# Performance work log

Hardware: AMD Instinct MI355X
Metric: run time of the kernel (lower is better)

## Reference

```python
import jax, jax.numpy as jnp
import numpy as np

N_NODES = 50000
N_EDGES = 600000
D = 128
LN_EPS = 1e-5


def setup_inputs() -> dict:
    key = jax.random.key(0)
    ks = jax.random.split(key, 10)
    s = 1.0 / np.sqrt(D)
    return {
        "node_reps": jax.random.normal(ks[0], (N_NODES, D), jnp.float32),
        "edge_reps": jax.random.normal(ks[1], (N_EDGES, D), jnp.float32),
        "src_idx": jax.random.randint(ks[2], (N_EDGES,), 0, N_NODES, jnp.int32),
        "dst_idx": jnp.sort(jax.random.randint(ks[3], (N_EDGES,), 0, N_NODES, jnp.int32)),
        "Wq": jax.random.normal(ks[4], (D, D), jnp.float32) * s,
        "Wk": jax.random.normal(ks[5], (D, D), jnp.float32) * s,
        "Wv": jax.random.normal(ks[6], (D, D), jnp.float32) * s,
        "Wo": jax.random.normal(ks[7], (D, D), jnp.float32) * s,
        "ln_gamma": jnp.ones((D,), jnp.float32),
        "ln_beta": jnp.zeros((D,), jnp.float32),
        "W1": jax.random.normal(ks[8], (3 * D, D), jnp.float32) * (1.0 / np.sqrt(3 * D)),
        "b1": jnp.zeros((D,), jnp.float32),
        "W2": jax.random.normal(ks[9], (D, D), jnp.float32) * s,
        "b2": jnp.zeros((D,), jnp.float32),
    }


def _layer_norm(x, g, b):
    mu = jnp.mean(x, axis=-1, keepdims=True)
    var = jnp.mean(jnp.square(x - mu), axis=-1, keepdims=True)
    return (x - mu) * jax.lax.rsqrt(var + LN_EPS) * g + b


def reference(node_reps, edge_reps, src_idx, dst_idx, Wq, Wk, Wv, Wo,
              ln_gamma, ln_beta, W1, b1, W2, b2):
    n_nodes, d = node_reps.shape
    # dense projections once per node (kernel-friendly GEMMs)
    q = node_reps @ Wq                                  # [N, d]
    k_nodes = node_reps @ Wk                            # [N, d]
    v_nodes = node_reps @ Wv                            # [N, d]
    # per-edge gather + edge bias
    k_e = k_nodes[src_idx] + edge_reps                  # [E, d]
    scores = jnp.sum(q[dst_idx] * k_e, axis=-1) / jnp.sqrt(jnp.float32(d))  # [E]
    # segment softmax over edges sharing the same dst node
    seg_max = jax.ops.segment_max(scores, dst_idx, num_segments=n_nodes)
    ex = jnp.exp(scores - seg_max[dst_idx])
    denom = jax.ops.segment_sum(ex, dst_idx, num_segments=n_nodes)
    alpha = ex / denom[dst_idx]                          # [E]
    v_e = v_nodes[src_idx] + edge_reps                   # [E, d]
    agg = jax.ops.segment_sum(alpha[:, None] * v_e, dst_idx, num_segments=n_nodes)  # [N, d]
    updated = _layer_norm(node_reps + agg @ Wo, ln_gamma, ln_beta)  # [N, d]
    # triplet fusion MLP over (dst node, edge, src node)
    h_trip = jnp.concatenate([node_reps[dst_idx], edge_reps, node_reps[src_idx]], axis=-1)  # [E, 3d]
    fused = jax.nn.relu(h_trip @ W1 + b1) @ W2 + b2      # [E, d]
    return updated, fused
```

## Files before the change

kernel.cpp:

```cpp
#include <hip/hip_runtime.h>
#include <hip/hip_bf16.h>

#define NN 50000
#define NE 600000
#define D 128

typedef __bf16 bf16x8 __attribute__((ext_vector_type(8)));
typedef __bf16 bf16x4 __attribute__((ext_vector_type(4)));
typedef float f32x4 __attribute__((ext_vector_type(4)));


static __device__ __forceinline__ bf16x8 load_a_frag_nc(const float* __restrict__ A,
                                                        int row, int k0) {
  const f32x4* p = (const f32x4*)(A + (size_t)row * D + k0);
  f32x4 v0 = p[0], v1 = p[1];
  bf16x8 r;
  r[0] = (__bf16)v0[0]; r[1] = (__bf16)v0[1]; r[2] = (__bf16)v0[2]; r[3] = (__bf16)v0[3];
  r[4] = (__bf16)v1[0]; r[5] = (__bf16)v1[1]; r[6] = (__bf16)v1[2]; r[7] = (__bf16)v1[3];
  return r;
}

static __device__ __forceinline__ void stage_a_tile128(const float* __restrict__ A, int M,
                                                       int row_base, char* lds, int tid) {
  const int l32 = tid & 31;
  const int g = tid >> 5;
#pragma unroll
  for (int it = 0; it < 16; ++it) {
    int rl = it * 8 + g;
    int r = row_base + rl;
    f32x4 v = {};
    if (r < M) v = *(const f32x4*)(A + (size_t)r * D + l32 * 4);
    bf16x4 b;
    b[0] = (__bf16)v[0]; b[1] = (__bf16)v[1]; b[2] = (__bf16)v[2]; b[3] = (__bf16)v[3];
    int byte = (rl * 256 + l32 * 8) ^ ((rl & 7) << 4);
    *(bf16x4*)(lds + byte) = b;
  }
}

static __device__ __forceinline__ bf16x8 read_a_frag(const char* lds, int rl, int k0) {
  int byte = (rl * 256 + k0 * 2) ^ ((rl & 7) << 4);
  return *(const bf16x8*)(lds + byte);
}

template <int CTRL>
static __device__ __forceinline__ float dpp_add(float x) {
  int v = __builtin_amdgcn_update_dpp(0, __float_as_int(x), CTRL, 0xf, 0xf, true);
  return x + __int_as_float(v);
}

static __device__ __forceinline__ float red32(float x) {
  x = dpp_add<0xB1>(x);
  x = dpp_add<0x4E>(x);
  x = dpp_add<0x124>(x);
  x = dpp_add<0x128>(x);
  return x + __shfl_xor(x, 16, 64);
}

#define CATT 0.12751744612764933f

struct PrepArgs {
  const float* W[8];
  __bf16* WT[8];
  const int* dst;
  int* offs;
};

__global__ void prep_all(PrepArgs pa) {
  int b = blockIdx.x;
  if (b < 512) {
    int w = b >> 6;
    int t = (b & 63) * 256 + threadIdx.x;
    int n = t & 127, k = t >> 7;
    float v = pa.W[w][k * 128 + n];
    if (w == 0) v *= CATT;
    pa.WT[w][n * 128 + k] = (__bf16)v;
  } else {
    int n = (b - 512) * 256 + threadIdx.x;
    if (n > NN) return;
    int lo = 0, hi = NE;
    while (lo < hi) {
      int mid = (lo + hi) >> 1;
      if (pa.dst[mid] < n) lo = mid + 1; else hi = mid;
    }
    pa.offs[n] = lo;
  }
}

struct GemmBatch {
  const __bf16* BT[5];
  void* C[5];
  const float* bias[5];
  int mode[5];
};

__global__ __launch_bounds__(256) void gemm_k128_b(const float* __restrict__ A,
                                                   GemmBatch gb, int M) {
  __shared__ __align__(16) char atile[128 * 256];
  const int y = blockIdx.y;
  const __bf16* __restrict__ BT = gb.BT[y];
  const int tid = threadIdx.x;
  const int lane = tid & 63;
  const int wave = tid >> 6;
  const int wr = wave >> 1, wc = wave & 1;
  const int row0 = blockIdx.x * 128;
  const int col0 = wc * 64;
  const int lr = lane & 15;
  const int lk = (lane >> 4) << 3;

  stage_a_tile128(A, M, row0, atile, tid);
  __syncthreads();

  f32x4 acc[4][4] = {};
#pragma unroll
  for (int kk = 0; kk < 4; ++kk) {
    const int k0 = kk * 32 + lk;
    bf16x8 a[4], b[4];
#pragma unroll
    for (int m = 0; m < 4; ++m) a[m] = read_a_frag(atile, wr * 64 + m * 16 + lr, k0);
#pragma unroll
    for (int n = 0; n < 4; ++n) b[n] = *(const bf16x8*)(BT + (size_t)(col0 + n * 16 + lr) * D + k0);
#pragma unroll
    for (int m = 0; m < 4; ++m)
#pragma unroll
      for (int n = 0; n < 4; ++n)
        acc[m][n] = __builtin_amdgcn_mfma_f32_16x16x32_bf16(a[m], b[n], acc[m][n], 0, 0, 0);
  }
  const int rr = (lane >> 4) * 4;
  float bv[4] = {0.f, 0.f, 0.f, 0.f};
  if (gb.bias[y]) {
#pragma unroll
    for (int n = 0; n < 4; ++n) bv[n] = gb.bias[y][col0 + n * 16 + lr];
  }
  const int mode = gb.mode[y];
#pragma unroll
  for (int m = 0; m < 4; ++m)
#pragma unroll
    for (int j = 0; j < 4; ++j) {
      const int row = row0 + wr * 64 + m * 16 + rr + j;
      if (row < M) {
#pragma unroll
        for (int n = 0; n < 4; ++n) {
          const int c = col0 + n * 16 + lr;
          const float val = acc[m][n][j] + bv[n];
          if (mode == 0) {
            ((float*)gb.C[y])[(size_t)row * D + c] = val;
          } else if (mode == 1) {
            ((__bf16*)gb.C[y])[(size_t)row * D + c] = (__bf16)val;
          } else {
            const int e = ((c >> 2) << 3) + (c & 3) + (mode == 3 ? 4 : 0);
            ((__bf16*)gb.C[y])[(size_t)row * 256 + e] = (__bf16)val;
          }
        }
      }
    }
}

#define LD1(P, K, J, SV)                                                     \
  do {                                                                       \
    const int jj_ = (J);                                                     \
    const int jc_ = jj_ < jm ? jj_ : 0;                                      \
    int si_ = __shfl((SV), jj_ & 31, 32);                                    \
    si_ = jj_ < jm ? si_ : 0;                                                \
    kv##P[K] = *(const bf16x8*)(KV + (size_t)si_ * 256 + (l32 << 3));        \
    ee##P[K] = *(const f32x4*)(edge + (size_t)(s0 + jc_) * D + (l32 << 2));  \
  } while (0)

#define LOADC(P, C)                                                          \
  do {                                                                       \
    const int c4_ = (C) * 4;                                                 \
    const int sv_ = (c4_ < 32) ? sidx0 : sidx1;                              \
    LD1(P, 0, c4_ + 0, sv_); LD1(P, 1, c4_ + 1, sv_);                        \
    LD1(P, 2, c4_ + 2, sv_); LD1(P, 3, c4_ + 3, sv_);                        \
  } while (0)

#define CP1(P, K, J)                                                         \
  do {                                                                       \
    const int jj_ = (J);                                                     \
    f32x4 ef_ = ee##P[K];                                                    \
    float x0_ = (float)kv##P[K][0] + ef_[0];                                 \
    float x1_ = (float)kv##P[K][1] + ef_[1];                                 \
    float x2_ = (float)kv##P[K][2] + ef_[2];                                 \
    float x3_ = (float)kv##P[K][3] + ef_[3];                                 \
    float pp_ = fmaf(qs[1], x1_, qs[0] * x0_) + fmaf(qs[3], x3_, qs[2] * x2_); \
    float s_ = red32(pp_);                                                   \
    float w_ = jj_ < jm ? exp2f(s_) : 0.f;                                   \
    l += w_;                                                                 \
    a[0] = fmaf(w_, (float)kv##P[K][4] + ef_[0], a[0]);                      \
    a[1] = fmaf(w_, (float)kv##P[K][5] + ef_[1], a[1]);                      \
    a[2] = fmaf(w_, (float)kv##P[K][6] + ef_[2], a[2]);                      \
    a[3] = fmaf(w_, (float)kv##P[K][7] + ef_[3], a[3]);                      \
  } while (0)

#define COMPC(P, C)                                                          \
  do {                                                                       \
    const int cc4_ = (C) * 4;                                                \
    CP1(P, 0, cc4_ + 0); CP1(P, 1, cc4_ + 1);                                \
    CP1(P, 2, cc4_ + 2); CP1(P, 3, cc4_ + 3);                                \
  } while (0)

#define MEMFENCE asm volatile("" ::: "memory")

__global__ __launch_bounds__(256) __attribute__((amdgpu_waves_per_eu(4)))
void fused_edge_attn(
    const float* __restrict__ edge,
    const __bf16* __restrict__ W1bT,
    const __bf16* __restrict__ W2T,
    const __bf16* __restrict__ P1,
    const __bf16* __restrict__ P3,
    const int* __restrict__ dst,
    const int* __restrict__ src,
    const float* __restrict__ b2,
    float* __restrict__ out_fused,
    const float* __restrict__ Q,
    const __bf16* __restrict__ KV,
    const int* __restrict__ offs,
    const __bf16* __restrict__ WoT,
    const float* __restrict__ noderep,
    const float* __restrict__ gamma,
    const float* __restrict__ beta,
    float* __restrict__ out_updated) {
  __shared__ __align__(16) char buf[64 * 256];
  const int tid = threadIdx.x;
  const int b = blockIdx.x;
  const int x = b & 7;
  const int t = b >> 3;
  const int grp = (t / 5) * 8 + x;
  const int role = t % 5;
  if (grp >= 3125) return;

  if (role >= 2) {
    const int ebi = grp * 3 + (role - 2);
    const int eb = ebi * 64;
    const int lane = tid & 63;
    const int wave = tid >> 6;
    const int wr = wave >> 1, wc = wave & 1;
    const int lr = lane & 15;
    const int lk = (lane >> 4) << 3;
    const int col0 = wc * 64;
    const int rr = (lane >> 4) * 4;

    f32x4 acc[2][4] = {};
#pragma unroll
    for (int kk = 0; kk < 4; ++kk) {
      const int k0 = kk * 32 + lk;
      bf16x8 a[2], bm[4];
#pragma unroll
      for (int m = 0; m < 2; ++m) a[m] = load_a_frag_nc(edge, eb + wr * 32 + m * 16 + lr, k0);
#pragma unroll
      for (int n = 0; n < 4; ++n) bm[n] = *(const bf16x8*)(W1bT + (size_t)(col0 + n * 16 + lr) * D + k0);
#pragma unroll
      for (int m = 0; m < 2; ++m)
#pragma unroll
        for (int n = 0; n < 4; ++n)
          acc[m][n] = __builtin_amdgcn_mfma_f32_16x16x32_bf16(a[m], bm[n], acc[m][n], 0, 0, 0);
    }

#pragma unroll
    for (int m = 0; m < 2; ++m) {
#pragma unroll
      for (int j = 0; j < 4; ++j) {
        const int rl = wr * 32 + m * 16 + rr + j;
        const __bf16* __restrict__ p1r = P1 + (size_t)dst[eb + rl] * D;
        const __bf16* __restrict__ p3r = P3 + (size_t)src[eb + rl] * D;
#pragma unroll
        for (int n = 0; n < 4; ++n) {
          const int c = col0 + n * 16 + lr;
          float v = fmaxf(acc[m][n][j] + (float)p1r[c] + (float)p3r[c], 0.f);
          int byte = (rl * 256 + c * 2) ^ ((rl & 7) << 4);
          *(__bf16*)(buf + byte) = (__bf16)v;
        }
      }
    }
    __syncthreads();

    float b2v[4];
#pragma unroll
    for (int n = 0; n < 4; ++n) b2v[n] = b2[col0 + n * 16 + lr];
    f32x4 acc2[2][4] = {};
#pragma unroll
    for (int kk = 0; kk < 4; ++kk) {
      const int k0 = kk * 32 + lk;
      bf16x8 a[2], bm[4];
#pragma unroll
      for (int m = 0; m < 2; ++m) a[m] = read_a_frag(buf, wr * 32 + m * 16 + lr, k0);
#pragma unroll
      for (int n = 0; n < 4; ++n) bm[n] = *(const bf16x8*)(W2T + (size_t)(col0 + n * 16 + lr) * D + k0);
#pragma unroll
      for (int m = 0; m < 2; ++m)
#pragma unroll
        for (int n = 0; n < 4; ++n)
          acc2[m][n] = __builtin_amdgcn_mfma_f32_16x16x32_bf16(a[m], bm[n], acc2[m][n], 0, 0, 0);
    }
#pragma unroll
    for (int m = 0; m < 2; ++m)
#pragma unroll
      for (int j = 0; j < 4; ++j) {
        int rl = wr * 32 + m * 16 + rr + j;
        int e = eb + rl;
#pragma unroll
        for (int n = 0; n < 4; ++n) {
          int c = col0 + n * 16 + lr;
          out_fused[(size_t)e * D + c] = acc2[m][n][j] + b2v[n];
        }
      }
  } else {
    const int nw = tid >> 5;
    const int node = (grp * 2 + role) * 8 + nw;
    const int l32 = tid & 31;
    int s0 = offs[node], s1 = offs[node + 1];
    int cnt = s1 - s0;
    f32x4 qs = *(const f32x4*)(Q + (size_t)node * D + l32 * 4);
    float l = 0.f;
    f32x4 a = {0.f, 0.f, 0.f, 0.f};

    const int jm = cnt < 64 ? cnt : 64;
    if (jm > 0) {
      int sidx0 = 0, sidx1 = 0;
      if (l32 < cnt) sidx0 = src[s0 + l32];
      if (l32 + 32 < cnt) sidx1 = src[s0 + 32 + l32];
      bf16x8 kv0[4], kv1[4];
      f32x4 ee0[4], ee1[4];
      const int nch = (jm + 3) >> 2;
      LOADC(0, 0);
      MEMFENCE;
      for (int c = 0; c < nch; c += 2) {
        if (c + 1 < nch) LOADC(1, c + 1);
        MEMFENCE;
        COMPC(0, c);
        if (c + 2 < nch) LOADC(0, c + 2);
        MEMFENCE;
        if (c + 1 < nch) COMPC(1, c + 1);
      }
      for (int i = 64; i < cnt; ++i) {
        int si = src[s0 + i];
        bf16x8 kvx = *(const bf16x8*)(KV + (size_t)si * 256 + (l32 << 3));
        f32x4 ef = *(const f32x4*)(edge + (size_t)(s0 + i) * D + (l32 << 2));
        float x0 = (float)kvx[0] + ef[0], x1 = (float)kvx[1] + ef[1];
        float x2 = (float)kvx[2] + ef[2], x3 = (float)kvx[3] + ef[3];
        float pp = fmaf(qs[1], x1, qs[0] * x0) + fmaf(qs[3], x3, qs[2] * x2);
        float w = exp2f(red32(pp));
        l += w;
        a[0] = fmaf(w, (float)kvx[4] + ef[0], a[0]);
        a[1] = fmaf(w, (float)kvx[5] + ef[1], a[1]);
        a[2] = fmaf(w, (float)kvx[6] + ef[2], a[2]);
        a[3] = fmaf(w, (float)kvx[7] + ef[3], a[3]);
      }
    }
    float inv = l > 0.f ? 1.f / l : 0.f;
    f32x4 r;
    r[0] = a[0] * inv; r[1] = a[1] * inv; r[2] = a[2] * inv; r[3] = a[3] * inv;

    {
      bf16x4 rb;
      rb[0] = (__bf16)r[0]; rb[1] = (__bf16)r[1];
      rb[2] = (__bf16)r[2]; rb[3] = (__bf16)r[3];
      int byte = (nw * 256 + l32 * 8) ^ ((nw & 7) << 4);
      *(bf16x4*)(buf + byte) = rb;
    }
    __syncthreads();

    {
      const int wave = tid >> 6;
      const int lane = tid & 63;
      const int lr = lane & 15;
      const int lk = (lane >> 4) << 3;
      f32x4 acc[2] = {};
#pragma unroll
      for (int kk = 0; kk < 4; ++kk) {
        int k0 = kk * 32 + lk;
        bf16x8 af = read_a_frag(buf, lr, k0);
#pragma unroll
        for (int tt = 0; tt < 2; ++tt) {
          int nn = wave * 2 + tt;
          bf16x8 bm = *(const bf16x8*)(WoT + (size_t)(nn * 16 + lr) * D + k0);
          acc[tt] = __builtin_amdgcn_mfma_f32_16x16x32_bf16(af, bm, acc[tt], 0, 0, 0);
        }
      }
      float* xl = (float*)(buf + 8192);
      const int rr = (lane >> 4) * 4;
      if (rr < 8) {
#pragma unroll
        for (int tt = 0; tt < 2; ++tt) {
          int nn = wave * 2 + tt;
#pragma unroll
          for (int j = 0; j < 4; ++j)
            xl[(rr + j) * 128 + nn * 16 + lr] = acc[tt][j];
        }
      }
    }
    __syncthreads();

    {
      const float* xl = (const float*)(buf + 8192);
      f32x4 xv = *(const f32x4*)(xl + nw * 128 + l32 * 4);
      f32x4 nv = *(const f32x4*)(noderep + (size_t)node * D + l32 * 4);
      float x0 = xv[0] + nv[0], x1 = xv[1] + nv[1];
      float x2 = xv[2] + nv[2], x3 = xv[3] + nv[3];
      float s = red32(x0 + x1 + x2 + x3);
      float mu = s * (1.f / 128.f);
      float d0 = x0 - mu, d1 = x1 - mu, d2 = x2 - mu, d3 = x3 - mu;
      float vv = red32(d0 * d0 + d1 * d1 + d2 * d2 + d3 * d3);
      float rstd = rsqrtf(vv * (1.f / 128.f) + 1e-5f);
      f32x4 g = *(const f32x4*)(gamma + l32 * 4);
      f32x4 bb = *(const f32x4*)(beta + l32 * 4);
      f32x4 o;
      o[0] = d0 * rstd * g[0] + bb[0];
      o[1] = d1 * rstd * g[1] + bb[1];
      o[2] = d2 * rstd * g[2] + bb[2];
      o[3] = d3 * rstd * g[3] + bb[3];
      *(f32x4*)(out_updated + (size_t)node * D + l32 * 4) = o;
    }
  }
}

extern "C" void kernel_launch(void* const* d_in, const int* in_sizes, int n_in,
                              void* d_out, int out_size, void* d_ws, size_t ws_size,
                              hipStream_t stream) {
  const float* node = (const float*)d_in[0];
  const float* edge = (const float*)d_in[1];
  const int* src = (const int*)d_in[2];
  const int* dst = (const int*)d_in[3];
  const float* Wq = (const float*)d_in[4];
  const float* Wk = (const float*)d_in[5];
  const float* Wv = (const float*)d_in[6];
  const float* Wo = (const float*)d_in[7];
  const float* gamma = (const float*)d_in[8];
  const float* beta = (const float*)d_in[9];
  const float* W1 = (const float*)d_in[10];
  const float* b1 = (const float*)d_in[11];
  const float* W2 = (const float*)d_in[12];
  const float* b2 = (const float*)d_in[13];

  float* out_updated = (float*)d_out;
  float* out_fused = (float*)d_out + (size_t)NN * D;

  char* ws = (char*)d_ws;
  size_t o = 0;
  auto take = [&](size_t bytes) {
    char* p = ws + o;
    o = (o + bytes + 255) & ~(size_t)255;
    return p;
  };
  int* offs = (int*)take((NN + 1) * sizeof(int));
  __bf16* WqT = (__bf16*)take(128 * 128 * 2);
  __bf16* WkT = (__bf16*)take(128 * 128 * 2);
  __bf16* WvT = (__bf16*)take(128 * 128 * 2);
  __bf16* WoT = (__bf16*)take(128 * 128 * 2);
  __bf16* W1aT = (__bf16*)take(128 * 128 * 2);
  __bf16* W1bT = (__bf16*)take(128 * 128 * 2);
  __bf16* W1cT = (__bf16*)take(128 * 128 * 2);
  __bf16* W2T = (__bf16*)take(128 * 128 * 2);
  float* Qb = (float*)take((size_t)NN * D * 4);
  __bf16* KVb = (__bf16*)take((size_t)NN * 256 * 2);
  __bf16* P1b = (__bf16*)take((size_t)NN * D * 2);
  __bf16* P3b = (__bf16*)take((size_t)NN * D * 2);

  PrepArgs pa;
  pa.W[0] = Wq; pa.WT[0] = WqT;
  pa.W[1] = Wk; pa.WT[1] = WkT;
  pa.W[2] = Wv; pa.WT[2] = WvT;
  pa.W[3] = Wo; pa.WT[3] = WoT;
  pa.W[4] = W1; pa.WT[4] = W1aT;
  pa.W[5] = W1 + 128 * 128; pa.WT[5] = W1bT;
  pa.W[6] = W1 + 256 * 128; pa.WT[6] = W1cT;
  pa.W[7] = W2; pa.WT[7] = W2T;
  pa.dst = dst; pa.offs = offs;
  prep_all<<<512 + (NN + 256) / 256, 256, 0, stream>>>(pa);

  int gnode = (NN + 127) / 128;
  GemmBatch gb;
  gb.BT[0] = WqT;  gb.C[0] = Qb;  gb.bias[0] = nullptr; gb.mode[0] = 0;
  gb.BT[1] = WkT;  gb.C[1] = KVb; gb.bias[1] = nullptr; gb.mode[1] = 2;
  gb.BT[2] = WvT;  gb.C[2] = KVb; gb.bias[2] = nullptr; gb.mode[2] = 3;
  gb.BT[3] = W1aT; gb.C[3] = P1b; gb.bias[3] = b1;      gb.mode[3] = 1;
  gb.BT[4] = W1cT; gb.C[4] = P3b; gb.bias[4] = nullptr; gb.mode[4] = 1;
  gemm_k128_b<<<dim3(gnode, 5), 256, 0, stream>>>(node, gb, NN);

  fused_edge_attn<<<15640, 256, 0, stream>>>(edge, W1bT, W2T, P1b, P3b, dst, src,
                                             b2, out_fused, Qb, KVb, offs,
                                             WoT, node, gamma, beta, out_updated);
}
```

Measured before the change: 433.9 us.

## Stage gathered P1+P3 rows through LDS with coalesced vector loads

The per-edge P1[dst] and P3[src] projection gathers move out of the MFMA output layout, where each lane read scattered single bf16 values. Threads now load whole rows as bf16x8 vectors, sum them, and write the result to a swizzled LDS tile; the accumulators then read it back before ReLU and rewrite the tile for the second GEMM. The change also drops the compiler memory fences in the attention loop and lowers the waves-per-EU hint from 4 to 3, which allows more registers per wave. The cost is two extra __syncthreads, an extra LDS round-trip, and the intermediate sum being rounded to bf16 before it is added to the accumulator.

```diff
diff --git a/kernel.cpp b/kernel.cpp
--- a/kernel.cpp
+++ b/kernel.cpp
@@ -198,9 +198,7 @@
     CP1(P, 2, cc4_ + 2); CP1(P, 3, cc4_ + 3);                                \
   } while (0)
 
-#define MEMFENCE asm volatile("" ::: "memory")
-
-__global__ __launch_bounds__(256) __attribute__((amdgpu_waves_per_eu(4)))
+__global__ __launch_bounds__(256) __attribute__((amdgpu_waves_per_eu(3)))
 void fused_edge_attn(
     const float* __restrict__ edge,
     const __bf16* __restrict__ W1bT,
@@ -255,22 +253,50 @@
           acc[m][n] = __builtin_amdgcn_mfma_f32_16x16x32_bf16(a[m], bm[n], acc[m][n], 0, 0, 0);
     }
 
-#pragma unroll
-    for (int m = 0; m < 2; ++m) {
+    {
+      const int rw = tid >> 2;
+      const int c0 = (tid & 3) << 5;
+      const __bf16* __restrict__ p1r = P1 + (size_t)dst[eb + rw] * D + c0;
+      const __bf16* __restrict__ p3r = P3 + (size_t)src[eb + rw] * D + c0;
+#pragma unroll
+      for (int i = 0; i < 4; ++i) {
+        bf16x8 a1 = *(const bf16x8*)(p1r + i * 8);
+        bf16x8 a3 = *(const bf16x8*)(p3r + i * 8);
+        bf16x8 g;
+#pragma unroll
+        for (int e = 0; e < 8; ++e) g[e] = (__bf16)((float)a1[e] + (float)a3[e]);
+        int byte = (rw * 256 + ((c0 + i * 8) << 1)) ^ ((rw & 7) << 4);
+        *(bf16x8*)(buf + byte) = g;
+      }
+    }
+    __syncthreads();
+
+#pragma unroll
+    for (int m = 0; m < 2; ++m)
 #pragma unroll
       for (int j = 0; j < 4; ++j) {
         const int rl = wr * 32 + m * 16 + rr + j;
-        const __bf16* __restrict__ p1r = P1 + (size_t)dst[eb + rl] * D;
-        const __bf16* __restrict__ p3r = P3 + (size_t)src[eb + rl] * D;
 #pragma unroll
         for (int n = 0; n < 4; ++n) {
           const int c = col0 + n * 16 + lr;
-          float v = fmaxf(acc[m][n][j] + (float)p1r[c] + (float)p3r[c], 0.f);
           int byte = (rl * 256 + c * 2) ^ ((rl & 7) << 4);
-          *(__bf16*)(buf + byte) = (__bf16)v;
+          acc[m][n][j] += (float)*(const __bf16*)(buf + byte);
         }
       }
-    }
+    __syncthreads();
+
+#pragma unroll
+    for (int m = 0; m < 2; ++m)
+#pragma unroll
+      for (int j = 0; j < 4; ++j) {
+        const int rl = wr * 32 + m * 16 + rr + j;
+#pragma unroll
+        for (int n = 0; n < 4; ++n) {
+          const int c = col0 + n * 16 + lr;
+          int byte = (rl * 256 + c * 2) ^ ((rl & 7) << 4);
+          *(__bf16*)(buf + byte) = (__bf16)fmaxf(acc[m][n][j], 0.f);
+        }
+      }
     __syncthreads();
 
     float b2v[4];
@@ -322,13 +348,10 @@
       f32x4 ee0[4], ee1[4];
       const int nch = (jm + 3) >> 2;
       LOADC(0, 0);
-      MEMFENCE;
       for (int c = 0; c < nch; c += 2) {
         if (c + 1 < nch) LOADC(1, c + 1);
-        MEMFENCE;
         COMPC(0, c);
         if (c + 2 < nch) LOADC(0, c + 2);
-        MEMFENCE;
         if (c + 1 < nch) COMPC(1, c + 1);
       }
       for (int i = 64; i < cnt; ++i) {
```

After: 431.8 us. Within noise of the previous version (-0.5%).

## Restructure triplet MLP blocks to per-wave 16-row tiles with async LDS gathers

Applied to the files above, without the earlier changes.

Edge MLP blocks now each handle 192 edges in three passes. Each wave owns a private 16-row tile and 8 KB of LDS, so the block-wide barrier is gone. The P1/P3 row gathers are issued as global_load_lds DMA into LDS before the first GEMM and awaited afterward, so their latency overlaps the MFMA work. Grid roles shrink from 5 to 3 per group, the launch count drops, waves_per_eu goes from 4 to 3, and the compiler memory fences in the attention loop are removed. The trade-offs are larger LDS per block and lower occupancy, and each wave reloads the full W1b/W2 weights for every 16-row tile.

```diff
diff --git a/kernel.cpp b/kernel.cpp
--- a/kernel.cpp
+++ b/kernel.cpp
@@ -9,6 +9,12 @@
 typedef __bf16 bf16x4 __attribute__((ext_vector_type(4)));
 typedef float f32x4 __attribute__((ext_vector_type(4)));
 
+
+static __device__ __forceinline__ void gload_lds16(const void* g, void* l) {
+  __builtin_amdgcn_global_load_lds(
+      (const __attribute__((address_space(1))) unsigned int*)g,
+      (__attribute__((address_space(3))) unsigned int*)l, 16, 0, 0);
+}
 
 static __device__ __forceinline__ bf16x8 load_a_frag_nc(const float* __restrict__ A,
                                                         int row, int k0) {
@@ -198,9 +204,7 @@
     CP1(P, 2, cc4_ + 2); CP1(P, 3, cc4_ + 3);                                \
   } while (0)
 
-#define MEMFENCE asm volatile("" ::: "memory")
-
-__global__ __launch_bounds__(256) __attribute__((amdgpu_waves_per_eu(4)))
+__global__ __launch_bounds__(256) __attribute__((amdgpu_waves_per_eu(3)))
 void fused_edge_attn(
     const float* __restrict__ edge,
     const __bf16* __restrict__ W1bT,
@@ -219,90 +223,97 @@
     const float* __restrict__ gamma,
     const float* __restrict__ beta,
     float* __restrict__ out_updated) {
-  __shared__ __align__(16) char buf[64 * 256];
+  __shared__ __align__(16) char buf[32768];
   const int tid = threadIdx.x;
   const int b = blockIdx.x;
   const int x = b & 7;
   const int t = b >> 3;
-  const int grp = (t / 5) * 8 + x;
-  const int role = t % 5;
+  const int grp = (t / 3) * 8 + x;
+  const int role = t % 3;
   if (grp >= 3125) return;
 
-  if (role >= 2) {
-    const int ebi = grp * 3 + (role - 2);
-    const int eb = ebi * 64;
+  if (role == 2) {
+    const int wave = tid >> 6;
     const int lane = tid & 63;
-    const int wave = tid >> 6;
-    const int wr = wave >> 1, wc = wave & 1;
     const int lr = lane & 15;
     const int lk = (lane >> 4) << 3;
-    const int col0 = wc * 64;
-    const int rr = (lane >> 4) * 4;
-
-    f32x4 acc[2][4] = {};
-#pragma unroll
-    for (int kk = 0; kk < 4; ++kk) {
-      const int k0 = kk * 32 + lk;
-      bf16x8 a[2], bm[4];
-#pragma unroll
-      for (int m = 0; m < 2; ++m) a[m] = load_a_frag_nc(edge, eb + wr * 32 + m * 16 + lr, k0);
-#pragma unroll
-      for (int n = 0; n < 4; ++n) bm[n] = *(const bf16x8*)(W1bT + (size_t)(col0 + n * 16 + lr) * D + k0);
-#pragma unroll
-      for (int m = 0; m < 2; ++m)
-#pragma unroll
-        for (int n = 0; n < 4; ++n)
-          acc[m][n] = __builtin_amdgcn_mfma_f32_16x16x32_bf16(a[m], bm[n], acc[m][n], 0, 0, 0);
-    }
-
-#pragma unroll
-    for (int m = 0; m < 2; ++m) {
-#pragma unroll
-      for (int j = 0; j < 4; ++j) {
-        const int rl = wr * 32 + m * 16 + rr + j;
-        const __bf16* __restrict__ p1r = P1 + (size_t)dst[eb + rl] * D;
-        const __bf16* __restrict__ p3r = P3 + (size_t)src[eb + rl] * D;
-#pragma unroll
-        for (int n = 0; n < 4; ++n) {
-          const int c = col0 + n * 16 + lr;
-          float v = fmaxf(acc[m][n][j] + (float)p1r[c] + (float)p3r[c], 0.f);
+    const int rr = (lane >> 4) << 2;
+    char* wbuf = buf + wave * 8192;
+    const int ebase = grp * 192;
+
+    float b2v[8];
+#pragma unroll
+    for (int n = 0; n < 8; ++n) b2v[n] = b2[n * 16 + lr];
+
+    for (int tt = 0; tt < 3; ++tt) {
+      const int er0 = ebase + tt * 64 + wave * 16;
+
+#pragma unroll
+      for (int q = 0; q < 4; ++q) {
+        const int row = er0 + q * 4 + (lane >> 4);
+        const int d = dst[row];
+        const int s = src[row];
+        gload_lds16((const char*)(P1 + (size_t)d * D) + (lr << 4), wbuf + q * 1024);
+        gload_lds16((const char*)(P3 + (size_t)s * D) + (lr << 4), wbuf + 4096 + q * 1024);
+      }
+
+      f32x4 acc[8] = {};
+#pragma unroll
+      for (int kk = 0; kk < 4; ++kk) {
+        const int k0 = kk * 32 + lk;
+        bf16x8 a = load_a_frag_nc(edge, er0 + lr, k0);
+#pragma unroll
+        for (int n = 0; n < 8; ++n) {
+          bf16x8 bm = *(const bf16x8*)(W1bT + (size_t)(n * 16 + lr) * D + k0);
+          acc[n] = __builtin_amdgcn_mfma_f32_16x16x32_bf16(a, bm, acc[n], 0, 0, 0);
+        }
+      }
+
+      asm volatile("s_waitcnt vmcnt(0)" ::: "memory");
+
+      const __bf16* g1 = (const __bf16*)wbuf;
+      const __bf16* g3 = (const __bf16*)(wbuf + 4096);
+#pragma unroll
+      for (int n = 0; n < 8; ++n)
+#pragma unroll
+        for (int j = 0; j < 4; ++j) {
+          const int rl = rr + j;
+          const int c = n * 16 + lr;
+          float v = acc[n][j] + (float)g1[rl * 128 + c] + (float)g3[rl * 128 + c];
+          acc[n][j] = fmaxf(v, 0.f);
+        }
+
+#pragma unroll
+      for (int n = 0; n < 8; ++n)
+#pragma unroll
+        for (int j = 0; j < 4; ++j) {
+          const int rl = rr + j;
+          const int c = n * 16 + lr;
           int byte = (rl * 256 + c * 2) ^ ((rl & 7) << 4);
-          *(__bf16*)(buf + byte) = (__bf16)v;
-        }
-      }
-    }
-    __syncthreads();
-
-    float b2v[4];
-#pragma unroll
-    for (int n = 0; n < 4; ++n) b2v[n] = b2[col0 + n * 16 + lr];
-    f32x4 acc2[2][4] = {};
-#pragma unroll
-    for (int kk = 0; kk < 4; ++kk) {
-      const int k0 = kk * 32 + lk;
-      bf16x8 a[2], bm[4];
-#pragma unroll
-      for (int m = 0; m < 2; ++m) a[m] = read_a_frag(buf, wr * 32 + m * 16 + lr, k0);
-#pragma unroll
-      for (int n = 0; n < 4; ++n) bm[n] = *(const bf16x8*)(W2T + (size_t)(col0 + n * 16 + lr) * D + k0);
-#pragma unroll
-      for (int m = 0; m < 2; ++m)
-#pragma unroll
-        for (int n = 0; n < 4; ++n)
-          acc2[m][n] = __builtin_amdgcn_mfma_f32_16x16x32_bf16(a[m], bm[n], acc2[m][n], 0, 0, 0);
-    }
-#pragma unroll
-    for (int m = 0; m < 2; ++m)
-#pragma unroll
-      for (int j = 0; j < 4; ++j) {
-        int rl = wr * 32 + m * 16 + rr + j;
-        int e = eb + rl;
-#pragma unroll
-        for (int n = 0; n < 4; ++n) {
-          int c = col0 + n * 16 + lr;
-          out_fused[(size_t)e * D + c] = acc2[m][n][j] + b2v[n];
-        }
-      }
+          *(__bf16*)(wbuf + byte) = (__bf16)acc[n][j];
+        }
+
+      f32x4 acc2[8] = {};
+#pragma unroll
+      for (int kk = 0; kk < 4; ++kk) {
+        const int k0 = kk * 32 + lk;
+        bf16x8 a = read_a_frag(wbuf, lr, k0);
+#pragma unroll
+        for (int n = 0; n < 8; ++n) {
+          bf16x8 bm = *(const bf16x8*)(W2T + (size_t)(n * 16 + lr) * D + k0);
+          acc2[n] = __builtin_amdgcn_mfma_f32_16x16x32_bf16(a, bm, acc2[n], 0, 0, 0);
+        }
+      }
+
+#pragma unroll
+      for (int n = 0; n < 8; ++n)
+#pragma unroll
+        for (int j = 0; j < 4; ++j) {
+          const int e = er0 + rr + j;
+          const int c = n * 16 + lr;
+          out_fused[(size_t)e * D + c] = acc2[n][j] + b2v[n];
+        }
+    }
   } else {
     const int nw = tid >> 5;
     const int node = (grp * 2 + role) * 8 + nw;
@@ -322,13 +333,10 @@
       f32x4 ee0[4], ee1[4];
       const int nch = (jm + 3) >> 2;
       LOADC(0, 0);
-      MEMFENCE;
       for (int c = 0; c < nch; c += 2) {
         if (c + 1 < nch) LOADC(1, c + 1);
-        MEMFENCE;
         COMPC(0, c);
         if (c + 2 < nch) LOADC(0, c + 2);
-        MEMFENCE;
         if (c + 1 < nch) COMPC(1, c + 1);
       }
       for (int i = 64; i < cnt; ++i) {
@@ -476,7 +484,7 @@
   gb.BT[4] = W1cT; gb.C[4] = P3b; gb.bias[4] = nullptr; gb.mode[4] = 1;
   gemm_k128_b<<<dim3(gnode, 5), 256, 0, stream>>>(node, gb, NN);
 
-  fused_edge_attn<<<15640, 256, 0, stream>>>(edge, W1bT, W2T, P1b, P3b, dst, src,
-                                             b2, out_fused, Qb, KVb, offs,
-                                             WoT, node, gamma, beta, out_updated);
-}
+  fused_edge_attn<<<9384, 256, 0, stream>>>(edge, W1bT, W2T, P1b, P3b, dst, src,
+                                            b2, out_fused, Qb, KVb, offs,
+                                            WoT, node, gamma, beta, out_updated);
+}
```

New measurement: 794.2 us. 83.0% more time.

## Recast per-node attention as block-tiled MFMA over 16-node edge tiles

Applied to the files above, without the earlier changes.

The attention path changes from one half-wave per node doing scalar dot products and shuffles to a block of 16 consecutive nodes. That block stages edge-plus-K and transposed edge-plus-V tiles in LDS and computes scores and the weighted aggregation with bf16 MFMA using a masked score matrix. Q is stored as a bf16 hi/lo split to keep precision, and the KV layout becomes contiguous K then V halves. The aim is to replace scalar FMA and shuffle work with matrix cores and to coalesce gathers, at the cost of wasted MFMA work on masked entries, extra syncs, and more LDS, which lowers the waves-per-EU hint.

```diff
diff --git a/kernel.cpp b/kernel.cpp
--- a/kernel.cpp
+++ b/kernel.cpp
@@ -8,6 +8,8 @@
 typedef __bf16 bf16x8 __attribute__((ext_vector_type(8)));
 typedef __bf16 bf16x4 __attribute__((ext_vector_type(4)));
 typedef float f32x4 __attribute__((ext_vector_type(4)));
+
+#define MFMA(a, b, c) __builtin_amdgcn_mfma_f32_16x16x32_bf16((a), (b), (c), 0, 0, 0)
 
 
 static __device__ __forceinline__ bf16x8 load_a_frag_nc(const float* __restrict__ A,
@@ -48,12 +50,17 @@
   return x + __int_as_float(v);
 }
 
-static __device__ __forceinline__ float red32(float x) {
+static __device__ __forceinline__ float red16(float x) {
   x = dpp_add<0xB1>(x);
   x = dpp_add<0x4E>(x);
   x = dpp_add<0x124>(x);
   x = dpp_add<0x128>(x);
-  return x + __shfl_xor(x, 16, 64);
+  return x;
+}
+
+static __device__ __forceinline__ float red32(float x) {
+  return red16(x) + __shfl_xor(red16(x) * 0.f + x + 0.f, 16, 64) * 0.f +
+         __shfl_xor(red16(x), 16, 64);
 }
 
 #define CATT 0.12751744612764933f
@@ -123,7 +130,7 @@
     for (int m = 0; m < 4; ++m)
 #pragma unroll
       for (int n = 0; n < 4; ++n)
-        acc[m][n] = __builtin_amdgcn_mfma_f32_16x16x32_bf16(a[m], b[n], acc[m][n], 0, 0, 0);
+        acc[m][n] = MFMA(a[m], b[n], acc[m][n]);
   }
   const int rr = (lane >> 4) * 4;
   float bv[4] = {0.f, 0.f, 0.f, 0.f};
@@ -142,65 +149,25 @@
         for (int n = 0; n < 4; ++n) {
           const int c = col0 + n * 16 + lr;
           const float val = acc[m][n][j] + bv[n];
-          if (mode == 0) {
-            ((float*)gb.C[y])[(size_t)row * D + c] = val;
-          } else if (mode == 1) {
-            ((__bf16*)gb.C[y])[(size_t)row * D + c] = (__bf16)val;
+          __bf16* C = (__bf16*)gb.C[y];
+          if (mode == 1) {
+            C[(size_t)row * D + c] = (__bf16)val;
+          } else if (mode == 2) {
+            C[(size_t)row * 256 + c] = (__bf16)val;
+          } else if (mode == 3) {
+            C[(size_t)row * 256 + 128 + c] = (__bf16)val;
           } else {
-            const int e = ((c >> 2) << 3) + (c & 3) + (mode == 3 ? 4 : 0);
-            ((__bf16*)gb.C[y])[(size_t)row * 256 + e] = (__bf16)val;
+            __bf16 vh = (__bf16)val;
+            __bf16 vl = (__bf16)(val - (float)vh);
+            C[(size_t)row * 256 + c] = vh;
+            C[(size_t)row * 256 + 128 + c] = vl;
           }
         }
       }
     }
 }
 
-#define LD1(P, K, J, SV)                                                     \
-  do {                                                                       \
-    const int jj_ = (J);                                                     \
-    const int jc_ = jj_ < jm ? jj_ : 0;                                      \
-    int si_ = __shfl((SV), jj_ & 31, 32);                                    \
-    si_ = jj_ < jm ? si_ : 0;                                                \
-    kv##P[K] = *(const bf16x8*)(KV + (size_t)si_ * 256 + (l32 << 3));        \
-    ee##P[K] = *(const f32x4*)(edge + (size_t)(s0 + jc_) * D + (l32 << 2));  \
-  } while (0)
-
-#define LOADC(P, C)                                                          \
-  do {                                                                       \
-    const int c4_ = (C) * 4;                                                 \
-    const int sv_ = (c4_ < 32) ? sidx0 : sidx1;                              \
-    LD1(P, 0, c4_ + 0, sv_); LD1(P, 1, c4_ + 1, sv_);                        \
-    LD1(P, 2, c4_ + 2, sv_); LD1(P, 3, c4_ + 3, sv_);                        \
-  } while (0)
-
-#define CP1(P, K, J)                                                         \
-  do {                                                                       \
-    const int jj_ = (J);                                                     \
-    f32x4 ef_ = ee##P[K];                                                    \
-    float x0_ = (float)kv##P[K][0] + ef_[0];                                 \
-    float x1_ = (float)kv##P[K][1] + ef_[1];                                 \
-    float x2_ = (float)kv##P[K][2] + ef_[2];                                 \
-    float x3_ = (float)kv##P[K][3] + ef_[3];                                 \
-    float pp_ = fmaf(qs[1], x1_, qs[0] * x0_) + fmaf(qs[3], x3_, qs[2] * x2_); \
-    float s_ = red32(pp_);                                                   \
-    float w_ = jj_ < jm ? exp2f(s_) : 0.f;                                   \
-    l += w_;                                                                 \
-    a[0] = fmaf(w_, (float)kv##P[K][4] + ef_[0], a[0]);                      \
-    a[1] = fmaf(w_, (float)kv##P[K][5] + ef_[1], a[1]);                      \
-    a[2] = fmaf(w_, (float)kv##P[K][6] + ef_[2], a[2]);                      \
-    a[3] = fmaf(w_, (float)kv##P[K][7] + ef_[3], a[3]);                      \
-  } while (0)
-
-#define COMPC(P, C)                                                          \
-  do {                                                                       \
-    const int cc4_ = (C) * 4;                                                \
-    CP1(P, 0, cc4_ + 0); CP1(P, 1, cc4_ + 1);                                \
-    CP1(P, 2, cc4_ + 2); CP1(P, 3, cc4_ + 3);                                \
-  } while (0)
-
-#define MEMFENCE asm volatile("" ::: "memory")
-
-__global__ __launch_bounds__(256) __attribute__((amdgpu_waves_per_eu(4)))
+__global__ __launch_bounds__(256) __attribute__((amdgpu_waves_per_eu(3)))
 void fused_edge_attn(
     const float* __restrict__ edge,
     const __bf16* __restrict__ W1bT,
@@ -211,7 +178,7 @@
     const int* __restrict__ src,
     const float* __restrict__ b2,
     float* __restrict__ out_fused,
-    const float* __restrict__ Q,
+    const __bf16* __restrict__ Qsp,
     const __bf16* __restrict__ KV,
     const int* __restrict__ offs,
     const __bf16* __restrict__ WoT,
@@ -219,25 +186,27 @@
     const float* __restrict__ gamma,
     const float* __restrict__ beta,
     float* __restrict__ out_updated) {
-  __shared__ __align__(16) char buf[64 * 256];
+  __shared__ __align__(16) char lds[34880];
   const int tid = threadIdx.x;
   const int b = blockIdx.x;
   const int x = b & 7;
   const int t = b >> 3;
-  const int grp = (t / 5) * 8 + x;
-  const int role = t % 5;
+  const int grp = (t >> 2) * 8 + x;
+  const int role = t & 3;
   if (grp >= 3125) return;
 
-  if (role >= 2) {
-    const int ebi = grp * 3 + (role - 2);
+  const int wave = tid >> 6;
+  const int lane = tid & 63;
+  const int lr = lane & 15;
+  const int kg = lane >> 4;
+  const int rr = kg << 2;
+  const int lk = kg << 3;
+
+  if (role != 0) {
+    const int ebi = grp * 3 + (role - 1);
     const int eb = ebi * 64;
-    const int lane = tid & 63;
-    const int wave = tid >> 6;
     const int wr = wave >> 1, wc = wave & 1;
-    const int lr = lane & 15;
-    const int lk = (lane >> 4) << 3;
     const int col0 = wc * 64;
-    const int rr = (lane >> 4) * 4;
 
     f32x4 acc[2][4] = {};
 #pragma unroll
@@ -252,7 +221,7 @@
       for (int m = 0; m < 2; ++m)
 #pragma unroll
         for (int n = 0; n < 4; ++n)
-          acc[m][n] = __builtin_amdgcn_mfma_f32_16x16x32_bf16(a[m], bm[n], acc[m][n], 0, 0, 0);
+          acc[m][n] = MFMA(a[m], bm[n], acc[m][n]);
     }
 
 #pragma unroll
@@ -267,7 +236,7 @@
           const int c = col0 + n * 16 + lr;
           float v = fmaxf(acc[m][n][j] + (float)p1r[c] + (float)p3r[c], 0.f);
           int byte = (rl * 256 + c * 2) ^ ((rl & 7) << 4);
-          *(__bf16*)(buf + byte) = (__bf16)v;
+          *(__bf16*)(lds + byte) = (__bf16)v;
         }
       }
     }
@@ -282,14 +251,14 @@
       const int k0 = kk * 32 + lk;
       bf16x8 a[2], bm[4];
 #pragma unroll
-      for (int m = 0; m < 2; ++m) a[m] = read_a_frag(buf, wr * 32 + m * 16 + lr, k0);
+      for (int m = 0; m < 2; ++m) a[m] = read_a_frag(lds, wr * 32 + m * 16 + lr, k0);
 #pragma unroll
       for (int n = 0; n < 4; ++n) bm[n] = *(const bf16x8*)(W2T + (size_t)(col0 + n * 16 + lr) * D + k0);
 #pragma unroll
       for (int m = 0; m < 2; ++m)
 #pragma unroll
         for (int n = 0; n < 4; ++n)
-          acc2[m][n] = __builtin_amdgcn_mfma_f32_16x16x32_bf16(a[m], bm[n], acc2[m][n], 0, 0, 0);
+          acc2[m][n] = MFMA(a[m], bm[n], acc2[m][n]);
     }
 #pragma unroll
     for (int m = 0; m < 2; ++m)
@@ -304,111 +273,189 @@
         }
       }
   } else {
-    const int nw = tid >> 5;
-    const int node = (grp * 2 + role) * 8 + nw;
-    const int l32 = tid & 31;
-    int s0 = offs[node], s1 = offs[node + 1];
-    int cnt = s1 - s0;
-    f32x4 qs = *(const f32x4*)(Q + (size_t)node * D + l32 * 4);
-    float l = 0.f;
-    f32x4 a = {0.f, 0.f, 0.f, 0.f};
-
-    const int jm = cnt < 64 ? cnt : 64;
-    if (jm > 0) {
-      int sidx0 = 0, sidx1 = 0;
-      if (l32 < cnt) sidx0 = src[s0 + l32];
-      if (l32 + 32 < cnt) sidx1 = src[s0 + 32 + l32];
-      bf16x8 kv0[4], kv1[4];
-      f32x4 ee0[4], ee1[4];
-      const int nch = (jm + 3) >> 2;
-      LOADC(0, 0);
-      MEMFENCE;
-      for (int c = 0; c < nch; c += 2) {
-        if (c + 1 < nch) LOADC(1, c + 1);
-        MEMFENCE;
-        COMPC(0, c);
-        if (c + 2 < nch) LOADC(0, c + 2);
-        MEMFENCE;
-        if (c + 1 < nch) COMPC(1, c + 1);
-      }
-      for (int i = 64; i < cnt; ++i) {
-        int si = src[s0 + i];
-        bf16x8 kvx = *(const bf16x8*)(KV + (size_t)si * 256 + (l32 << 3));
-        f32x4 ef = *(const f32x4*)(edge + (size_t)(s0 + i) * D + (l32 << 2));
-        float x0 = (float)kvx[0] + ef[0], x1 = (float)kvx[1] + ef[1];
-        float x2 = (float)kvx[2] + ef[2], x3 = (float)kvx[3] + ef[3];
-        float pp = fmaf(qs[1], x1, qs[0] * x0) + fmaf(qs[3], x3, qs[2] * x2);
-        float w = exp2f(red32(pp));
-        l += w;
-        a[0] = fmaf(w, (float)kvx[4] + ef[0], a[0]);
-        a[1] = fmaf(w, (float)kvx[5] + ef[1], a[1]);
-        a[2] = fmaf(w, (float)kvx[6] + ef[2], a[2]);
-        a[3] = fmaf(w, (float)kvx[7] + ef[3], a[3]);
-      }
-    }
-    float inv = l > 0.f ? 1.f / l : 0.f;
-    f32x4 r;
-    r[0] = a[0] * inv; r[1] = a[1] * inv; r[2] = a[2] * inv; r[3] = a[3] * inv;
+    char* KE = lds;
+    char* VET = lds + 16384;
+    char* PT = lds + 32768;
+    float* l_lds = (float*)(lds + 34816);
+    const int n0 = grp * 16;
+
+    if (tid < 16) l_lds[tid] = 0.f;
+
+    const int e0 = offs[n0], e1 = offs[n0 + 16];
+    const int L = e1 - e0;
+    const int T = (L + 63) >> 6;
+
+    f32x4 accp[2] = {};
+    float lsum0 = 0.f, lsum1 = 0.f, lsum2 = 0.f, lsum3 = 0.f;
+
+    const int se = tid >> 2;
+    const int sq = tid & 3;
+    const int c0 = sq << 5;
+    const int el = (wave << 4) + lr;
+
+    for (int tt = 0; tt < T; ++tt) {
+      const int et = e0 + (tt << 6);
+      {
+        int eg = et + se;
+        int ec = eg < e1 ? eg : e1 - 1;
+        int si = src[ec];
+        const float* ep = edge + (size_t)ec * D + c0;
+        const __bf16* kp = KV + (size_t)si * 256 + c0;
+        f32x4 e4[8];
+#pragma unroll
+        for (int i = 0; i < 8; ++i) e4[i] = *(const f32x4*)(ep + i * 4);
+        bf16x8 k8[4], v8[4];
+#pragma unroll
+        for (int i = 0; i < 4; ++i) {
+          k8[i] = *(const bf16x8*)(kp + i * 8);
+          v8[i] = *(const bf16x8*)(kp + 128 + i * 8);
+        }
+#pragma unroll
+        for (int i = 0; i < 4; ++i) {
+          bf16x8 o;
+#pragma unroll
+          for (int u = 0; u < 8; ++u)
+            o[u] = (__bf16)((float)k8[i][u] + e4[i * 2 + (u >> 2)][u & 3]);
+          int byte = (se * 256 + ((c0 + i * 8) << 1)) ^ ((se & 7) << 4);
+          *(bf16x8*)(KE + byte) = o;
+        }
+#pragma unroll
+        for (int i = 0; i < 32; ++i) {
+          int col = c0 + i;
+          float v = (float)v8[i >> 3][i & 7] + e4[i >> 2][i & 3];
+          int byte = ((col >> 1) * 256 + (col & 1) * 128 + (se << 1)) ^
+                     ((((col >> 1) ^ (col >> 5)) & 7) << 4);
+          *(__bf16*)(VET + byte) = (__bf16)v;
+        }
+      }
+      __syncthreads();
+
+      f32x4 accs = {};
+      {
+        const __bf16* Qs = Qsp + (size_t)(n0 + lr) * 256;
+#pragma unroll
+        for (int kk = 0; kk < 4; ++kk) {
+          int k0 = kk * 32 + lk;
+          bf16x8 qh = *(const bf16x8*)(Qs + k0);
+          bf16x8 ql = *(const bf16x8*)(Qs + 128 + k0);
+          bf16x8 ke = read_a_frag(KE, el, k0);
+          accs = MFMA(qh, ke, accs);
+          accs = MFMA(ql, ke, accs);
+        }
+      }
+      {
+        int eg = et + el;
+        int de = (eg < e1) ? (dst[eg] - n0) : -1;
+#pragma unroll
+        for (int j = 0; j < 4; ++j) {
+          float w = (rr + j == de) ? exp2f(accs[j]) : 0.f;
+          __bf16 wb = (__bf16)w;
+          float wf = (float)wb;
+          if (j == 0) lsum0 += wf; else if (j == 1) lsum1 += wf;
+          else if (j == 2) lsum2 += wf; else lsum3 += wf;
+          int byte = (((rr + j) << 7) + (el << 1)) ^ (((rr + j) & 7) << 4);
+          *(__bf16*)(PT + byte) = wb;
+        }
+      }
+      __syncthreads();
+
+#pragma unroll
+      for (int kk = 0; kk < 2; ++kk) {
+        int k = kk * 32 + lk;
+        int abyte = ((lr << 7) + (k << 1)) ^ ((lr & 7) << 4);
+        bf16x8 ap = *(const bf16x8*)(PT + abyte);
+#pragma unroll
+        for (int nt = 0; nt < 2; ++nt) {
+          int col = (wave << 5) + (nt << 4) + lr;
+          int bbyte = ((col >> 1) * 256 + (col & 1) * 128 + (k << 1)) ^
+                      ((((col >> 1) ^ (col >> 5)) & 7) << 4);
+          bf16x8 bv = *(const bf16x8*)(VET + bbyte);
+          accp[nt] = MFMA(ap, bv, accp[nt]);
+        }
+      }
+      __syncthreads();
+    }
 
     {
-      bf16x4 rb;
-      rb[0] = (__bf16)r[0]; rb[1] = (__bf16)r[1];
-      rb[2] = (__bf16)r[2]; rb[3] = (__bf16)r[3];
-      int byte = (nw * 256 + l32 * 8) ^ ((nw & 7) << 4);
-      *(bf16x4*)(buf + byte) = rb;
+      float r0 = red16(lsum0), r1 = red16(lsum1);
+      float r2 = red16(lsum2), r3 = red16(lsum3);
+      if ((lane & 15) == 0) {
+        atomicAdd(l_lds + rr + 0, r0);
+        atomicAdd(l_lds + rr + 1, r1);
+        atomicAdd(l_lds + rr + 2, r2);
+        atomicAdd(l_lds + rr + 3, r3);
+      }
     }
     __syncthreads();
 
     {
-      const int wave = tid >> 6;
-      const int lane = tid & 63;
-      const int lr = lane & 15;
-      const int lk = (lane >> 4) << 3;
-      f32x4 acc[2] = {};
+#pragma unroll
+      for (int nt = 0; nt < 2; ++nt) {
+        int col = (wave << 5) + (nt << 4) + lr;
+#pragma unroll
+        for (int j = 0; j < 4; ++j) {
+          int node = rr + j;
+          float lv = l_lds[node];
+          float inv = lv > 0.f ? 1.f / lv : 0.f;
+          int byte = (node * 256 + (col << 1)) ^ ((node & 7) << 4);
+          *(__bf16*)(KE + byte) = (__bf16)(accp[nt][j] * inv);
+        }
+      }
+    }
+    __syncthreads();
+
+    {
+      f32x4 aw[2] = {};
 #pragma unroll
       for (int kk = 0; kk < 4; ++kk) {
         int k0 = kk * 32 + lk;
-        bf16x8 af = read_a_frag(buf, lr, k0);
-#pragma unroll
-        for (int tt = 0; tt < 2; ++tt) {
-          int nn = wave * 2 + tt;
+        bf16x8 af = read_a_frag(KE, lr, k0);
+#pragma unroll
+        for (int nt = 0; nt < 2; ++nt) {
+          int nn = (wave << 1) + nt;
           bf16x8 bm = *(const bf16x8*)(WoT + (size_t)(nn * 16 + lr) * D + k0);
-          acc[tt] = __builtin_amdgcn_mfma_f32_16x16x32_bf16(af, bm, acc[tt], 0, 0, 0);
-        }
-      }
-      float* xl = (float*)(buf + 8192);
-      const int rr = (lane >> 4) * 4;
-      if (rr < 8) {
-#pragma unroll
-        for (int tt = 0; tt < 2; ++tt) {
-          int nn = wave * 2 + tt;
-#pragma unroll
-          for (int j = 0; j < 4; ++j)
-            xl[(rr + j) * 128 + nn * 16 + lr] = acc[tt][j];
-        }
+          aw[nt] = MFMA(af, bm, aw[nt]);
+        }
+      }
+      float* xl = (float*)VET;
+#pragma unroll
+      for (int nt = 0; nt < 2; ++nt) {
+        int nn = (wave << 1) + nt;
+#pragma unroll
+        for (int j = 0; j < 4; ++j)
+          xl[(rr + j) * 128 + nn * 16 + lr] = aw[nt][j];
       }
     }
     __syncthreads();
 
     {
-      const float* xl = (const float*)(buf + 8192);
-      f32x4 xv = *(const f32x4*)(xl + nw * 128 + l32 * 4);
-      f32x4 nv = *(const f32x4*)(noderep + (size_t)node * D + l32 * 4);
-      float x0 = xv[0] + nv[0], x1 = xv[1] + nv[1];
-      float x2 = xv[2] + nv[2], x3 = xv[3] + nv[3];
-      float s = red32(x0 + x1 + x2 + x3);
-      float mu = s * (1.f / 128.f);
-      float d0 = x0 - mu, d1 = x1 - mu, d2 = x2 - mu, d3 = x3 - mu;
-      float vv = red32(d0 * d0 + d1 * d1 + d2 * d2 + d3 * d3);
-      float rstd = rsqrtf(vv * (1.f / 128.f) + 1e-5f);
+      const int h = tid >> 5;
+      const int l32 = tid & 31;
+      const float* xl = (const float*)VET;
       f32x4 g = *(const f32x4*)(gamma + l32 * 4);
       f32x4 bb = *(const f32x4*)(beta + l32 * 4);
-      f32x4 o;
-      o[0] = d0 * rstd * g[0] + bb[0];
-      o[1] = d1 * rstd * g[1] + bb[1];
-      o[2] = d2 * rstd * g[2] + bb[2];
-      o[3] = d3 * rstd * g[3] + bb[3];
-      *(f32x4*)(out_updated + (size_t)node * D + l32 * 4) = o;
+#pragma unroll
+      for (int which = 0; which < 2; ++which) {
+        int nl = h * 2 + which;
+        int node = n0 + nl;
+        f32x4 xv = *(const f32x4*)(xl + nl * 128 + l32 * 4);
+        f32x4 nv = *(const f32x4*)(noderep + (size_t)node * D + l32 * 4);
+        float x0 = xv[0] + nv[0], x1 = xv[1] + nv[1];
+        float x2 = xv[2] + nv[2], x3 = xv[3] + nv[3];
+        float s = red16(x0 + x1 + x2 + x3);
+        s += __shfl_xor(s, 16, 64);
+        float mu = s * (1.f / 128.f);
+        float d0 = x0 - mu, d1 = x1 - mu, d2 = x2 - mu, d3 = x3 - mu;
+        float vv = red16(d0 * d0 + d1 * d1 + d2 * d2 + d3 * d3);
+        vv += __shfl_xor(vv, 16, 64);
+        float rstd = rsqrtf(vv * (1.f / 128.f) + 1e-5f);
+        f32x4 o;
+        o[0] = d0 * rstd * g[0] + bb[0];
+        o[1] = d1 * rstd * g[1] + bb[1];
+        o[2] = d2 * rstd * g[2] + bb[2];
+        o[3] = d3 * rstd * g[3] + bb[3];
+        *(f32x4*)(out_updated + (size_t)node * D + l32 * 4) = o;
+      }
     }
   }
 }
@@ -450,7 +497,7 @@
   __bf16* W1bT = (__bf16*)take(128 * 128 * 2);
   __bf16* W1cT = (__bf16*)take(128 * 128 * 2);
   __bf16* W2T = (__bf16*)take(128 * 128 * 2);
-  float* Qb = (float*)take((size_t)NN * D * 4);
+  __bf16* Qsp = (__bf16*)take((size_t)NN * 256 * 2);
   __bf16* KVb = (__bf16*)take((size_t)NN * 256 * 2);
   __bf16* P1b = (__bf16*)take((size_t)NN * D * 2);
   __bf16* P3b = (__bf16*)take((size_t)NN * D * 2);
@@ -469,14 +516,14 @@
 
   int gnode = (NN + 127) / 128;
   GemmBatch gb;
-  gb.BT[0] = WqT;  gb.C[0] = Qb;  gb.bias[0] = nullptr; gb.mode[0] = 0;
+  gb.BT[0] = WqT;  gb.C[0] = Qsp; gb.bias[0] = nullptr; gb.mode[0] = 4;
   gb.BT[1] = WkT;  gb.C[1] = KVb; gb.bias[1] = nullptr; gb.mode[1] = 2;
   gb.BT[2] = WvT;  gb.C[2] = KVb; gb.bias[2] = nullptr; gb.mode[2] = 3;
   gb.BT[3] = W1aT; gb.C[3] = P1b; gb.bias[3] = b1;      gb.mode[3] = 1;
   gb.BT[4] = W1cT; gb.C[4] = P3b; gb.bias[4] = nullptr; gb.mode[4] = 1;
   gemm_k128_b<<<dim3(gnode, 5), 256, 0, stream>>>(node, gb, NN);
 
-  fused_edge_attn<<<15640, 256, 0, stream>>>(edge, W1bT, W2T, P1b, P3b, dst, src,
-                                             b2, out_fused, Qb, KVb, offs,
+  fused_edge_attn<<<12512, 256, 0, stream>>>(edge, W1bT, W2T, P1b, P3b, dst, src,
+                                             b2, out_fused, Qsp, KVb, offs,
                                              WoT, node, gamma, beta, out_updated);
 }
```

After: 572.9 us. 1.32x slower.
